# Performance work log

Hardware: AMD Instinct MI355X
Metric: run time of the kernel (lower is better)

The kernel has to match this reference:

```python
import jax, jax.numpy as jnp
import numpy as np

EMBED = 256

def _resize(x, h, w):
    # bilinear, half-pixel centers == torch align_corners=False
    B, C = x.shape[:2]
    return jax.image.resize(x, (B, C, h, w), method='bilinear')

def _conv(x, w, b, pad):
    y = jax.lax.conv_general_dilated(x, w, (1, 1), [(pad, pad), (pad, pad)],
                                     dimension_numbers=('NCHW', 'OIHW', 'NCHW'))
    return y + b[None, :, None, None]

def _box1d(x, r, axis):
    # windowed sum over [i-r, i+r], window clipped at borders
    x = jnp.moveaxis(x, axis, -1)
    n = x.shape[-1]
    c = jnp.cumsum(x, axis=-1)
    idx = jnp.arange(n)
    hi = c[..., jnp.clip(idx + r, 0, n - 1)]
    lo_i = idx - r - 1
    lo = jnp.where(lo_i >= 0, c[..., jnp.clip(lo_i, 0, n - 1)], 0.0)
    return jnp.moveaxis(hi - lo, -1, axis)

def _box_mean(x, r):
    # mean filter over (2r+1)^2 window, normalized by valid pixel count at borders
    H, W = x.shape[-2:]
    s = _box1d(_box1d(x, r, -2), r, -1)
    ch = _box1d(jnp.ones((H,), x.dtype), r, 0)
    cw = _box1d(jnp.ones((W,), x.dtype), r, 0)
    return s / (ch[:, None] * cw[None, :])

def _guided_filter(I, p, r, eps):
    # He et al. guided filter. I: (H,W) guide, p: (C,H,W) src, vectorized over C
    mean_I = _box_mean(I, r)
    var_I = _box_mean(I * I, r) - mean_I ** 2
    mean_p = _box_mean(p, r)
    cov_Ip = _box_mean(I[None] * p, r) - mean_I[None] * mean_p
    a = cov_Ip / (var_I[None] + eps)
    b = mean_p - a * mean_I[None]
    return _box_mean(a, r) * I[None] + _box_mean(b, r)

def _forward(fg, bg, mask, feat, w1, b1, w2, b2, w3, b3, wm, bm):
    h2, w2d = 2 * mask.shape[2], 2 * mask.shape[3]
    mask_2x_raw = _resize(mask, h2, w2d)
    feat_2x_raw = _resize(feat, h2, w2d)
    fg_2x = _resize(fg, h2, w2d)
    bg_2x = _resize(bg, h2, w2d)
    x = jnp.concatenate((mask_2x_raw, fg_2x, bg_2x, feat_2x_raw), axis=1)
    x = jax.nn.relu(_conv(x, w1, b1, 0))
    feat_2x = jax.nn.relu(_conv(x, w2, b2, 2))
    guide = jnp.mean(fg_2x, axis=1)[0] * 128.0  # (H2, W2)
    r = int(0.01 * h2)  # static shape -> python int, jit-safe
    filt = _guided_filter(guide, feat_2x[0], r, 0.01)[None]  # (1,C,H2,W2)
    feat_2x = jax.nn.relu(_conv(filt, w3, b3, 0))
    mask_2x = jax.nn.sigmoid(_conv(feat_2x, wm, bm, 0))
    return mask_2x, feat_2x

def setup_inputs():
    key = jax.random.key(0)
    ks = jax.random.split(key, 8)
    E = EMBED
    return {
        'fg': jax.random.normal(ks[0], (1, 3, 128, 128), jnp.float32),
        'bg': jax.random.normal(ks[1], (1, 3, 128, 128), jnp.float32),
        'mask': jax.random.uniform(ks[2], (1, 1, 128, 128), dtype=jnp.float32),
        'feat': jax.random.normal(ks[3], (1, E, 128, 128), jnp.float32),
        'w1': jax.random.normal(ks[4], (E, E + 7, 1, 1), jnp.float32) * 0.05,
        'b1': jnp.zeros((E,), jnp.float32),
        'w2': jax.random.normal(ks[5], (E, E, 5, 5), jnp.float32) * 0.02,
        'b2': jnp.zeros((E,), jnp.float32),
        'w3': jax.random.normal(ks[6], (E, E, 1, 1), jnp.float32) * 0.05,
        'b3': jnp.zeros((E,), jnp.float32),
        'wm': jax.random.normal(ks[7], (1, E, 1, 1), jnp.float32) * 0.05,
        'bm': jnp.zeros((1,), jnp.float32),
    }

def reference(fg, bg, mask, feat, w1, b1, w2, b2, w3, b3, wm, bm):
    return _forward(fg, bg, mask, feat, w1, b1, w2, b2, w3, b3, wm, bm)
```

## Files before the change

### kernel.cpp

```cpp
#include <hip/hip_runtime.h>
#include <hip/hip_bf16.h>
#include <math.h>


#define P2 65536
#define PADW 260

typedef short  frag8  __attribute__((ext_vector_type(8)));
typedef float  f32x4  __attribute__((ext_vector_type(4)));

__device__ __forceinline__ void load16_lds(const void* gsrc, void* lds) {
    __builtin_amdgcn_global_load_lds((const __attribute__((address_space(1))) void*)gsrc,
                                     (__attribute__((address_space(3))) void*)lds, 16, 0, 0);
}

struct BilC { int y0, y1, x0, x1; float wy0, wy1, wx0, wx1; };
__device__ __forceinline__ BilC bil_coords(int oy, int ox) {
    BilC c;
    int m = oy >> 1;
    if ((oy & 1) == 0) { c.y0 = (m > 0) ? m - 1 : 0; c.y1 = m; c.wy0 = 0.25f; }
    else               { c.y0 = m; c.y1 = (m < 127) ? m + 1 : 127; c.wy0 = 0.75f; }
    c.wy1 = 1.0f - c.wy0;
    int n = ox >> 1;
    if ((ox & 1) == 0) { c.x0 = (n > 0) ? n - 1 : 0; c.x1 = n; c.wx0 = 0.25f; }
    else               { c.x0 = n; c.x1 = (n < 127) ? n + 1 : 127; c.wx0 = 0.75f; }
    c.wx1 = 1.0f - c.wx0;
    return c;
}
__device__ __forceinline__ float bil_eval(const float* __restrict__ src, const BilC& c) {
    return c.wy0 * (c.wx0 * src[c.y0 * 128 + c.x0] + c.wx1 * src[c.y0 * 128 + c.x1])
         + c.wy1 * (c.wx0 * src[c.y1 * 128 + c.x0] + c.wx1 * src[c.y1 * 128 + c.x1]);
}

__global__ void upsample_x(const float* __restrict__ mask, const float* __restrict__ fg,
                           const float* __restrict__ bg, const float* __restrict__ feat,
                           __hip_bfloat16* __restrict__ xp) {
    int p = blockIdx.x * 256 + threadIdx.x;
    int chunk = blockIdx.y;
    union { __hip_bfloat16 h[8]; f32x4 v; } u;
    if (chunk >= 33) {
        f32x4 z = {0.f, 0.f, 0.f, 0.f};
        *(f32x4*)&xp[((size_t)chunk * P2 + p) * 8] = z;
        return;
    }
    BilC bc = bil_coords(p >> 8, p & 255);
#pragma unroll
    for (int j = 0; j < 8; j++) {
        int c = chunk * 8 + j;
        float v = 0.f;
        if (c < 263) {
            const float* src = (c == 0) ? mask
                             : (c < 4)  ? fg + (c - 1) * 16384
                             : (c < 7)  ? bg + (c - 4) * 16384
                             :            feat + (c - 7) * 16384;
            v = bil_eval(src, bc);
        }
        u.h[j] = __float2bfloat16(v);
    }
    *(f32x4*)&xp[((size_t)chunk * P2 + p) * 8] = u.v;
}

__global__ void guide_make(const float* __restrict__ fg, float* __restrict__ guide) {
    int p = blockIdx.x * 256 + threadIdx.x;
    BilC bc = bil_coords(p >> 8, p & 255);
    float s = bil_eval(fg, bc) + bil_eval(fg + 16384, bc) + bil_eval(fg + 32768, bc);
    guide[p] = s * (128.0f / 3.0f);
}

__global__ void gf_stats(const float* __restrict__ guide, float* __restrict__ meanI,
                         float* __restrict__ varI) {
    int p = blockIdx.x * 256 + threadIdx.x;
    int y = p >> 8, xq = p & 255;
    int y0 = (y - 2 > 0) ? y - 2 : 0, y1 = (y + 2 < 255) ? y + 2 : 255;
    int x0 = (xq - 2 > 0) ? xq - 2 : 0, x1 = (xq + 2 < 255) ? xq + 2 : 255;
    float s = 0.f, ss = 0.f;
    for (int yy = y0; yy <= y1; yy++)
        for (int xx = x0; xx <= x1; xx++) {
            float v = guide[yy * 256 + xx];
            s += v; ss += v * v;
        }
    float inv = 1.0f / (float)((y1 - y0 + 1) * (x1 - x0 + 1));
    float m = s * inv;
    meanI[p] = m;
    varI[p] = ss * inv - m * m;
}

__global__ void border_zero(__hip_bfloat16* __restrict__ y1p) {
    int idx = blockIdx.x * 256 + threadIdx.x;
    int p = idx >> 4;
    if (p >= PADW * PADW) return;
    int py = p / PADW, px = p - py * PADW;
    if (py >= 2 && py < 258 && px >= 2 && px < 258) return;
    f32x4 z = {0.f, 0.f, 0.f, 0.f};
    f32x4* dst = (f32x4*)&y1p[(size_t)p * 256 + (idx & 15) * 16];
    dst[0] = z; dst[1] = z;
}

__global__ void repack_1x1(const float* __restrict__ W, __hip_bfloat16* __restrict__ dst,
                           int K, int KT) {
    int idx = blockIdx.x * 256 + threadIdx.x;
    if (idx >= KT * 16 * 64) return;
    int lane = idx & 63;
    int nbg = (idx >> 6) & 15;
    int kt = idx >> 10;
    int oc = nbg * 16 + (lane & 15);
    int ic0 = kt * 32 + (lane >> 4) * 8;
    union { __hip_bfloat16 h[8]; f32x4 v; } u;
#pragma unroll
    for (int j = 0; j < 8; j++) {
        int ic = ic0 + j;
        u.h[j] = (ic < K) ? __float2bfloat16(W[(size_t)oc * K + ic]) : __float2bfloat16(0.f);
    }
    *(f32x4*)&dst[(size_t)idx * 8] = u.v;
}

__global__ void repack_w2(const float* __restrict__ w2, __hip_bfloat16* __restrict__ wpk) {
    int idx = blockIdx.x * 256 + threadIdx.x;
    int lane = idx & 63;
    int nb = (idx >> 6) & 15;
    int kt = (idx >> 10) & 7;
    int t  = idx >> 13;
    int oc = nb * 16 + (lane & 15);
    int ic0 = kt * 32 + (lane >> 4) * 8;
    union { __hip_bfloat16 h[8]; f32x4 v; } u;
#pragma unroll
    for (int j = 0; j < 8; j++)
        u.h[j] = __float2bfloat16(w2[(oc * 256 + ic0 + j) * 25 + t]);
    *(f32x4*)&wpk[(size_t)idx * 8] = u.v;
}

template<int MODE>
__global__ __launch_bounds__(256) void mfma_1x1(const __hip_bfloat16* __restrict__ xch,
                                                const __hip_bfloat16* __restrict__ wpk,
                                                const float* __restrict__ bias,
                                                void* __restrict__ outp, int KT) {
    __shared__ __align__(16) __hip_bfloat16 Asm[2][128 * 32];
    __shared__ __align__(16) __hip_bfloat16 Bsm[2][8 * 64 * 8];
    const int tid = threadIdx.x;
    const int wave = tid >> 6, lane = tid & 63;
    const int q = lane >> 4, m16 = lane & 15;
    const int wm = wave & 1, wn = wave >> 1;
    const int pb = blockIdx.x * 128, oh = blockIdx.y;

    f32x4 acc[4][4] = {};

    auto stA = [&](int kt, int buf) {
#pragma unroll
        for (int it = 0; it < 2; it++) {
            int chb = it * 256 + wave * 64;
            int ch = chb + lane;
            int px = ch >> 2, oct = ch & 3;
            const __hip_bfloat16* src = xch + ((size_t)(kt * 4 + oct) * P2 + pb + px) * 8;
            load16_lds(src, &Asm[buf][chb * 8]);
        }
    };
    auto stB = [&](int kt, int buf) {
#pragma unroll
        for (int it = 0; it < 2; it++) {
            int chb = it * 256 + wave * 64;
            int ch = chb + lane;
            int nb = ch >> 6, l = ch & 63;
            const __hip_bfloat16* src = wpk + (((size_t)kt * 16 + oh * 8 + nb) * 64 + l) * 8;
            load16_lds(src, &Bsm[buf][chb * 8]);
        }
    };
    stA(0, 0); stB(0, 0);
    int buf = 0;
    for (int kt = 0; kt < KT; kt++) {
        __syncthreads();
        if (kt + 1 < KT) { stA(kt + 1, buf ^ 1); stB(kt + 1, buf ^ 1); }
        frag8 a[4], b[4];
#pragma unroll
        for (int i = 0; i < 4; i++)
            a[i] = *(const frag8*)&Asm[buf][((wm * 4 + i) * 16 + m16) * 32 + q * 8];
#pragma unroll
        for (int j = 0; j < 4; j++)
            b[j] = *(const frag8*)&Bsm[buf][((wn * 4 + j) * 64 + lane) * 8];
#pragma unroll
        for (int i = 0; i < 4; i++)
#pragma unroll
            for (int j = 0; j < 4; j++)
                acc[i][j] = __builtin_amdgcn_mfma_f32_16x16x32_bf16(a[i], b[j], acc[i][j], 0, 0, 0);
        buf ^= 1;
    }
    if (MODE == 0) {
        __hip_bfloat16* y1p = (__hip_bfloat16*)outp;
#pragma unroll
        for (int j = 0; j < 4; j++) {
            int oc = oh * 128 + (wn * 4 + j) * 16 + m16;
            float bj = bias[oc];
#pragma unroll
            for (int i = 0; i < 4; i++) {
                f32x4 v = acc[i][j];
#pragma unroll
                for (int e = 0; e < 4; e++) {
                    int pix = pb + (wm * 4 + i) * 16 + q * 4 + e;
                    int py = pix >> 8, px = pix & 255;
                    float tv = v[e] + bj;
                    y1p[((size_t)(py + 2) * PADW + px + 2) * 256 + oc] =
                        __float2bfloat16(tv > 0.f ? tv : 0.f);
                }
            }
        }
    } else {
        float* out = (float*)outp;
#pragma unroll
        for (int j = 0; j < 4; j++) {
            int oc = oh * 128 + (wn * 4 + j) * 16 + m16;
            float bj = bias[oc];
#pragma unroll
            for (int i = 0; i < 4; i++) {
                f32x4 v = acc[i][j];
#pragma unroll
                for (int e = 0; e < 4; e++) { float tv = v[e] + bj; v[e] = tv > 0.f ? tv : 0.f; }
                *(f32x4*)&out[(size_t)oc * P2 + pb + (wm * 4 + i) * 16 + q * 4] = v;
            }
        }
    }
}

__global__ __launch_bounds__(128, 2) void conv5x5_mfma(const __hip_bfloat16* __restrict__ y1p,
                                                       const __hip_bfloat16* __restrict__ wpk,
                                                       const float* __restrict__ bias,
                                                       float* __restrict__ out) {
    __shared__ __align__(16) __hip_bfloat16 Asm[2][12 * 20 * 32];
    const int tid = threadIdx.x;
    const int wave = tid >> 6;
    const int lane = tid & 63;
    const int q = lane >> 4;
    const int m16 = lane & 15;
    const int bx = blockIdx.x, by = blockIdx.y, oh = blockIdx.z;

    f32x4 acc[4][8] = {};

    auto stageA = [&](int ict, int buf) {
#pragma unroll
        for (int g = 0; g < 8; g++) {
            int grp = g * 2 + wave;
            if (grp >= 15) break;
            int chb = grp * 64;
            int ch = chb + lane;
            int oct = ch & 3, pl = ch >> 2;
            int pc = pl % 20, pr = pl / 20;
            const __hip_bfloat16* src =
                y1p + (size_t)((by * 8 + pr) * PADW + bx * 16 + pc) * 256 + ict * 32 + oct * 8;
            load16_lds(src, &Asm[buf][chb * 8]);
        }
    };
    auto loadB = [&](int s, frag8* dst) {
        int ict = s / 25, tap = s - ict * 25;
        const __hip_bfloat16* base =
            wpk + ((size_t)((tap * 8 + ict) * 16 + oh * 8) * 64 + lane) * 8;
#pragma unroll
        for (int j = 0; j < 8; j++)
            dst[j] = *(const frag8*)(base + (size_t)j * 512);
    };

    frag8 bA[8], bB[8];
    stageA(0, 0);
    loadB(0, bA);
    int abuf = 0;

    auto step = [&](int s, frag8* bcur, frag8* bnxt) {
        int ict = s / 25, tap = s - ict * 25;
        if (tap == 0) __syncthreads();
        if (s + 1 < 200) loadB(s + 1, bnxt);
        if (tap == 24 && ict < 7) stageA(ict + 1, abuf ^ 1);
        int dy = tap / 5, dx = tap - dy * 5;
        frag8 a[4];
#pragma unroll
        for (int i = 0; i < 4; i++)
            a[i] = *(const frag8*)&Asm[abuf][((wave * 4 + i + dy) * 20 + m16 + dx) * 32 + q * 8];
#pragma unroll
        for (int i = 0; i < 4; i++)
#pragma unroll
            for (int j = 0; j < 8; j++)
                acc[i][j] = __builtin_amdgcn_mfma_f32_16x16x32_bf16(a[i], bcur[j], acc[i][j], 0, 0, 0);
        if (tap == 24) abuf ^= 1;
    };
    for (int s = 0; s < 200; s += 2) { step(s, bA, bB); step(s + 1, bB, bA); }

#pragma unroll
    for (int j = 0; j < 8; j++) {
        int oc = oh * 128 + j * 16 + m16;
        float bj = bias[oc];
#pragma unroll
        for (int i = 0; i < 4; i++) {
            int r = wave * 4 + i;
            f32x4 v = acc[i][j];
#pragma unroll
            for (int e = 0; e < 4; e++) {
                float t = v[e] + bj;
                v[e] = (t > 0.f) ? t : 0.f;
            }
            *(f32x4*)&out[(size_t)oc * P2 + (by * 8 + r) * 256 + bx * 16 + q * 4] = v;
        }
    }
}

__global__ __launch_bounds__(256) void gf_stream(const float* __restrict__ p,
                                                 const float* __restrict__ guide,
                                                 const float* __restrict__ meanI,
                                                 const float* __restrict__ varI,
                                                 __hip_bfloat16* __restrict__ filt) {
    __shared__ float Prow[260], IProw[260], Arow[260], Brow[260];
    const int t = threadIdx.x;
    const int c = blockIdx.y;
    const int Y0 = blockIdx.x * 64;
    const float* pc = p + (size_t)c * P2;
    if (t < 4) {
        int e = (t < 2) ? t : 256 + t;
        Prow[e] = 0.f; IProw[e] = 0.f; Arow[e] = 0.f; Brow[e] = 0.f;
    }
    int xlo = (t - 2 > 0) ? t - 2 : 0, xhi = (t + 2 < 255) ? t + 2 : 255;
    const float cxr = 1.0f / (float)(xhi - xlo + 1);
    float hp[5] = {0, 0, 0, 0, 0}, hip[5] = {0, 0, 0, 0, 0};
    float ha[5] = {0, 0, 0, 0, 0}, hb[5] = {0, 0, 0, 0, 0};
    float vp = 0.f, vip = 0.f, va = 0.f, vb = 0.f;
    __syncthreads();
    for (int s = 0; s < 72; s++) {
        int yL = Y0 - 4 + s;
        bool okL = ((unsigned)yL < 256u);
        if (okL) {
            float pv = pc[yL * 256 + t];
            Prow[t + 2] = pv;
            IProw[t + 2] = guide[yL * 256 + t] * pv;
        }
        __syncthreads();
        float hpn = 0.f, hipn = 0.f;
        if (okL) {
            hpn  = Prow[t] + Prow[t + 1] + Prow[t + 2] + Prow[t + 3] + Prow[t + 4];
            hipn = IProw[t] + IProw[t + 1] + IProw[t + 2] + IProw[t + 3] + IProw[t + 4];
        }
        vp += hpn - hp[0];  vip += hipn - hip[0];
        hp[0] = hp[1]; hp[1] = hp[2]; hp[2] = hp[3]; hp[3] = hp[4]; hp[4] = hpn;
        hip[0] = hip[1]; hip[1] = hip[2]; hip[2] = hip[3]; hip[3] = hip[4]; hip[4] = hipn;
        int yA = yL - 2;
        float aV = 0.f, bV = 0.f;
        if ((unsigned)yA < 256u && yA >= Y0 - 2) {
            int ylo = (yA - 2 > 0) ? yA - 2 : 0, yhi = (yA + 2 < 255) ? yA + 2 : 255;
            float inv1 = cxr / (float)(yhi - ylo + 1);
            float mI = meanI[yA * 256 + t], vI = varI[yA * 256 + t];
            float mp = vp * inv1, mip = vip * inv1;
            float cov = mip - mI * mp;
            aV = cov / (vI + 0.01f);
            bV = mp - aV * mI;
        }
        Arow[t + 2] = aV;
        Brow[t + 2] = bV;
        __syncthreads();
        float han = Arow[t] + Arow[t + 1] + Arow[t + 2] + Arow[t + 3] + Arow[t + 4];
        float hbn = Brow[t] + Brow[t + 1] + Brow[t + 2] + Brow[t + 3] + Brow[t + 4];
        va += han - ha[0];  vb += hbn - hb[0];
        ha[0] = ha[1]; ha[1] = ha[2]; ha[2] = ha[3]; ha[3] = ha[4]; ha[4] = han;
        hb[0] = hb[1]; hb[1] = hb[2]; hb[2] = hb[3]; hb[3] = hb[4]; hb[4] = hbn;
        int yo = yL - 4;
        if (yo >= Y0 && yo < Y0 + 64 && (unsigned)yo < 256u) {
            int ylo = (yo - 2 > 0) ? yo - 2 : 0, yhi = (yo + 2 < 255) ? yo + 2 : 255;
            float inv2 = cxr / (float)(yhi - ylo + 1);
            float I = guide[yo * 256 + t];
            filt[(size_t)c * P2 + yo * 256 + t] = __float2bfloat16((va * I + vb) * inv2);
        }
    }
}

__global__ void transpose_cp(const __hip_bfloat16* __restrict__ filt,
                             __hip_bfloat16* __restrict__ filtp) {
    __shared__ __hip_bfloat16 T[8][1024];
    int tid = threadIdx.x;
    int p0 = blockIdx.x * 1024;
    int cg = blockIdx.y;
    for (int i = tid; i < 8192; i += 256) {
        int r = i >> 10, pl = i & 1023;
        T[r][pl] = filt[(size_t)(cg * 8 + r) * P2 + p0 + pl];
    }
    __syncthreads();
    for (int pl = tid; pl < 1024; pl += 256) {
        union { __hip_bfloat16 h[8]; f32x4 v; } u;
#pragma unroll
        for (int j = 0; j < 8; j++) u.h[j] = T[j][pl];
        *(f32x4*)&filtp[((size_t)cg * P2 + p0 + pl) * 8] = u.v;
    }
}

__global__ void mask_head(const float* __restrict__ feat, const float* __restrict__ wm,
                          const float* __restrict__ bm, float* __restrict__ out) {
    int p = blockIdx.x * 256 + threadIdx.x;
    float acc = bm[0];
    for (int c = 0; c < 256; c++) acc += wm[c] * feat[(size_t)c * P2 + p];
    out[p] = 1.0f / (1.0f + expf(-acc));
}

extern "C" void kernel_launch(void* const* d_in, const int* in_sizes, int n_in,
                              void* d_out, int out_size, void* d_ws, size_t ws_size,
                              hipStream_t stream) {
    const float* fg   = (const float*)d_in[0];
    const float* bg   = (const float*)d_in[1];
    const float* mask = (const float*)d_in[2];
    const float* feat = (const float*)d_in[3];
    const float* w1   = (const float*)d_in[4];
    const float* b1   = (const float*)d_in[5];
    const float* w2   = (const float*)d_in[6];
    const float* b2   = (const float*)d_in[7];
    const float* w3   = (const float*)d_in[8];
    const float* b3   = (const float*)d_in[9];
    const float* wm   = (const float*)d_in[10];
    const float* bm   = (const float*)d_in[11];
    float* out = (float*)d_out;
    char* w8 = (char*)d_ws;

    float* pbuf = (float*)w8;
    __hip_bfloat16* xp    = (__hip_bfloat16*)(w8 + 67108864);
    __hip_bfloat16* filt  = (__hip_bfloat16*)(w8 + 67108864);
    __hip_bfloat16* filtp = (__hip_bfloat16*)w8;
    __hip_bfloat16* y1p   = (__hip_bfloat16*)(w8 + 104857600);
    __hip_bfloat16* wpk2  = (__hip_bfloat16*)(w8 + 139468800);
    __hip_bfloat16* wpk1  = (__hip_bfloat16*)(w8 + 142745600);
    __hip_bfloat16* wpk3  = (__hip_bfloat16*)(w8 + 142893056);
    float* guide = (float*)(w8 + 143024128);
    float* meanI = guide + P2;
    float* varI  = meanI + P2;

    upsample_x<<<dim3(256, 36), 256, 0, stream>>>(mask, fg, bg, feat, xp);
    guide_make<<<256, 256, 0, stream>>>(fg, guide);
    gf_stats<<<256, 256, 0, stream>>>(guide, meanI, varI);
    border_zero<<<4225, 256, 0, stream>>>(y1p);
    repack_w2<<<800, 256, 0, stream>>>(w2, wpk2);
    repack_1x1<<<36, 256, 0, stream>>>(w1, wpk1, 263, 9);
    repack_1x1<<<32, 256, 0, stream>>>(w3, wpk3, 256, 8);
    mfma_1x1<0><<<dim3(512, 2), 256, 0, stream>>>(xp, wpk1, b1, y1p, 9);
    conv5x5_mfma<<<dim3(16, 32, 2), 128, 0, stream>>>(y1p, wpk2, b2, pbuf);
    gf_stream<<<dim3(4, 256), 256, 0, stream>>>(pbuf, guide, meanI, varI, filt);
    transpose_cp<<<dim3(64, 32), 256, 0, stream>>>(filt, filtp);
    mfma_1x1<1><<<dim3(512, 2), 256, 0, stream>>>(filtp, wpk3, b3, out + P2, 8);
    mask_head<<<256, 256, 0, stream>>>(out + P2, wm, bm, out);
}
```

Baseline: 459.4 us.

## Fuse prep kernels, stage conv1 output via LDS, store conv5x5 output as fp16

Merges the border-zero and three weight-repack kernels into one launch. The first 1x1 conv epilogue now stages its tile in LDS so it can write 16-byte coalesced rows into the padded NHWC buffer instead of scattered 2-byte stores. The 5x5 conv writes its activation in fp16 rather than fp32, halving the traffic into the guided filter, and the mask head is vectorised to four pixels per thread. The fp16 intermediate adds rounding error before the guided filter.

```diff
diff --git a/kernel.cpp b/kernel.cpp
--- a/kernel.cpp
+++ b/kernel.cpp
@@ -1,5 +1,6 @@
 #include <hip/hip_runtime.h>
 #include <hip/hip_bf16.h>
+#include <hip/hip_fp16.h>
 #include <math.h>
 
 
@@ -85,48 +86,52 @@
     varI[p] = ss * inv - m * m;
 }
 
-__global__ void border_zero(__hip_bfloat16* __restrict__ y1p) {
-    int idx = blockIdx.x * 256 + threadIdx.x;
-    int p = idx >> 4;
-    if (p >= PADW * PADW) return;
-    int py = p / PADW, px = p - py * PADW;
-    if (py >= 2 && py < 258 && px >= 2 && px < 258) return;
-    f32x4 z = {0.f, 0.f, 0.f, 0.f};
-    f32x4* dst = (f32x4*)&y1p[(size_t)p * 256 + (idx & 15) * 16];
-    dst[0] = z; dst[1] = z;
-}
-
-__global__ void repack_1x1(const float* __restrict__ W, __hip_bfloat16* __restrict__ dst,
-                           int K, int KT) {
-    int idx = blockIdx.x * 256 + threadIdx.x;
-    if (idx >= KT * 16 * 64) return;
-    int lane = idx & 63;
-    int nbg = (idx >> 6) & 15;
-    int kt = idx >> 10;
-    int oc = nbg * 16 + (lane & 15);
-    int ic0 = kt * 32 + (lane >> 4) * 8;
-    union { __hip_bfloat16 h[8]; f32x4 v; } u;
-#pragma unroll
-    for (int j = 0; j < 8; j++) {
-        int ic = ic0 + j;
-        u.h[j] = (ic < K) ? __float2bfloat16(W[(size_t)oc * K + ic]) : __float2bfloat16(0.f);
-    }
-    *(f32x4*)&dst[(size_t)idx * 8] = u.v;
-}
-
-__global__ void repack_w2(const float* __restrict__ w2, __hip_bfloat16* __restrict__ wpk) {
-    int idx = blockIdx.x * 256 + threadIdx.x;
-    int lane = idx & 63;
-    int nb = (idx >> 6) & 15;
-    int kt = (idx >> 10) & 7;
-    int t  = idx >> 13;
-    int oc = nb * 16 + (lane & 15);
-    int ic0 = kt * 32 + (lane >> 4) * 8;
-    union { __hip_bfloat16 h[8]; f32x4 v; } u;
-#pragma unroll
-    for (int j = 0; j < 8; j++)
-        u.h[j] = __float2bfloat16(w2[(oc * 256 + ic0 + j) * 25 + t]);
-    *(f32x4*)&wpk[(size_t)idx * 8] = u.v;
+__global__ void prep_all(const float* __restrict__ w2, const float* __restrict__ w1,
+                         const float* __restrict__ w3,
+                         __hip_bfloat16* __restrict__ wpk2, __hip_bfloat16* __restrict__ wpk1,
+                         __hip_bfloat16* __restrict__ wpk3, __hip_bfloat16* __restrict__ y1p) {
+    int b = blockIdx.x;
+    int tid = threadIdx.x;
+    if (b < 4225) {
+        int idx = b * 256 + tid;
+        int p = idx >> 4;
+        if (p >= PADW * PADW) return;
+        int py = p / PADW, px = p - py * PADW;
+        if (py >= 2 && py < 258 && px >= 2 && px < 258) return;
+        f32x4 z = {0.f, 0.f, 0.f, 0.f};
+        f32x4* dst = (f32x4*)&y1p[(size_t)p * 256 + (idx & 15) * 16];
+        dst[0] = z; dst[1] = z;
+    } else if (b < 5025) {
+        int idx = (b - 4225) * 256 + tid;
+        int lane = idx & 63;
+        int nb = (idx >> 6) & 15;
+        int kt = (idx >> 10) & 7;
+        int t  = idx >> 13;
+        int oc = nb * 16 + (lane & 15);
+        int ic0 = kt * 32 + (lane >> 4) * 8;
+        union { __hip_bfloat16 h[8]; f32x4 v; } u;
+#pragma unroll
+        for (int j = 0; j < 8; j++)
+            u.h[j] = __float2bfloat16(w2[(oc * 256 + ic0 + j) * 25 + t]);
+        *(f32x4*)&wpk2[(size_t)idx * 8] = u.v;
+    } else {
+        const float* W; __hip_bfloat16* dst; int K, KT, idx;
+        if (b < 5061) { W = w1; dst = wpk1; K = 263; KT = 9; idx = (b - 5025) * 256 + tid; }
+        else          { W = w3; dst = wpk3; K = 256; KT = 8; idx = (b - 5061) * 256 + tid; }
+        if (idx >= KT * 16 * 64) return;
+        int lane = idx & 63;
+        int nbg = (idx >> 6) & 15;
+        int kt = idx >> 10;
+        int oc = nbg * 16 + (lane & 15);
+        int ic0 = kt * 32 + (lane >> 4) * 8;
+        union { __hip_bfloat16 h[8]; f32x4 v; } u;
+#pragma unroll
+        for (int j = 0; j < 8; j++) {
+            int ic = ic0 + j;
+            u.h[j] = (ic < K) ? __float2bfloat16(W[(size_t)oc * K + ic]) : __float2bfloat16(0.f);
+        }
+        *(f32x4*)&dst[(size_t)idx * 8] = u.v;
+    }
 }
 
 template<int MODE>
@@ -134,8 +139,9 @@
                                                 const __hip_bfloat16* __restrict__ wpk,
                                                 const float* __restrict__ bias,
                                                 void* __restrict__ outp, int KT) {
-    __shared__ __align__(16) __hip_bfloat16 Asm[2][128 * 32];
-    __shared__ __align__(16) __hip_bfloat16 Bsm[2][8 * 64 * 8];
+    __shared__ __align__(16) char smem[MODE == 0 ? 34816 : 32768];
+    __hip_bfloat16* Asm0 = (__hip_bfloat16*)smem;
+    __hip_bfloat16* Bsm0 = (__hip_bfloat16*)(smem + 16384);
     const int tid = threadIdx.x;
     const int wave = tid >> 6, lane = tid & 63;
     const int q = lane >> 4, m16 = lane & 15;
@@ -151,7 +157,7 @@
             int ch = chb + lane;
             int px = ch >> 2, oct = ch & 3;
             const __hip_bfloat16* src = xch + ((size_t)(kt * 4 + oct) * P2 + pb + px) * 8;
-            load16_lds(src, &Asm[buf][chb * 8]);
+            load16_lds(src, &Asm0[(size_t)buf * 4096 + chb * 8]);
         }
     };
     auto stB = [&](int kt, int buf) {
@@ -161,7 +167,7 @@
             int ch = chb + lane;
             int nb = ch >> 6, l = ch & 63;
             const __hip_bfloat16* src = wpk + (((size_t)kt * 16 + oh * 8 + nb) * 64 + l) * 8;
-            load16_lds(src, &Bsm[buf][chb * 8]);
+            load16_lds(src, &Bsm0[(size_t)buf * 4096 + chb * 8]);
         }
     };
     stA(0, 0); stB(0, 0);
@@ -172,10 +178,10 @@
         frag8 a[4], b[4];
 #pragma unroll
         for (int i = 0; i < 4; i++)
-            a[i] = *(const frag8*)&Asm[buf][((wm * 4 + i) * 16 + m16) * 32 + q * 8];
+            a[i] = *(const frag8*)&Asm0[(size_t)buf * 4096 + ((wm * 4 + i) * 16 + m16) * 32 + q * 8];
 #pragma unroll
         for (int j = 0; j < 4; j++)
-            b[j] = *(const frag8*)&Bsm[buf][((wn * 4 + j) * 64 + lane) * 8];
+            b[j] = *(const frag8*)&Bsm0[(size_t)buf * 4096 + ((wn * 4 + j) * 64 + lane) * 8];
 #pragma unroll
         for (int i = 0; i < 4; i++)
 #pragma unroll
@@ -184,7 +190,36 @@
         buf ^= 1;
     }
     if (MODE == 0) {
+        __syncthreads();
+        __hip_bfloat16* Ct = (__hip_bfloat16*)smem;
+#pragma unroll
+        for (int j = 0; j < 4; j++) {
+            int ocr = (wn * 4 + j) * 16 + m16;
+            float bj = bias[oh * 128 + ocr];
+#pragma unroll
+            for (int i = 0; i < 4; i++) {
+                f32x4 v = acc[i][j];
+#pragma unroll
+                for (int e = 0; e < 4; e++) {
+                    int pxr = (wm * 4 + i) * 16 + q * 4 + e;
+                    float tv = v[e] + bj;
+                    Ct[pxr * 136 + ocr] = __float2bfloat16(tv > 0.f ? tv : 0.f);
+                }
+            }
+        }
+        __syncthreads();
         __hip_bfloat16* y1p = (__hip_bfloat16*)outp;
+        int colr = (tid & 15) * 8;
+#pragma unroll
+        for (int it = 0; it < 8; it++) {
+            int pxr = it * 16 + (tid >> 4);
+            int pix = pb + pxr;
+            int py = pix >> 8, px = pix & 255;
+            f32x4 val = *(f32x4*)&Ct[pxr * 136 + colr];
+            *(f32x4*)&y1p[((size_t)(py + 2) * PADW + px + 2) * 256 + oh * 128 + colr] = val;
+        }
+    } else {
+        float* out = (float*)outp;
 #pragma unroll
         for (int j = 0; j < 4; j++) {
             int oc = oh * 128 + (wn * 4 + j) * 16 + m16;
@@ -193,25 +228,6 @@
             for (int i = 0; i < 4; i++) {
                 f32x4 v = acc[i][j];
 #pragma unroll
-                for (int e = 0; e < 4; e++) {
-                    int pix = pb + (wm * 4 + i) * 16 + q * 4 + e;
-                    int py = pix >> 8, px = pix & 255;
-                    float tv = v[e] + bj;
-                    y1p[((size_t)(py + 2) * PADW + px + 2) * 256 + oc] =
-                        __float2bfloat16(tv > 0.f ? tv : 0.f);
-                }
-            }
-        }
-    } else {
-        float* out = (float*)outp;
-#pragma unroll
-        for (int j = 0; j < 4; j++) {
-            int oc = oh * 128 + (wn * 4 + j) * 16 + m16;
-            float bj = bias[oc];
-#pragma unroll
-            for (int i = 0; i < 4; i++) {
-                f32x4 v = acc[i][j];
-#pragma unroll
                 for (int e = 0; e < 4; e++) { float tv = v[e] + bj; v[e] = tv > 0.f ? tv : 0.f; }
                 *(f32x4*)&out[(size_t)oc * P2 + pb + (wm * 4 + i) * 16 + q * 4] = v;
             }
@@ -222,7 +238,7 @@
 __global__ __launch_bounds__(128, 2) void conv5x5_mfma(const __hip_bfloat16* __restrict__ y1p,
                                                        const __hip_bfloat16* __restrict__ wpk,
                                                        const float* __restrict__ bias,
-                                                       float* __restrict__ out) {
+                                                       __half* __restrict__ pf) {
     __shared__ __align__(16) __hip_bfloat16 Asm[2][12 * 20 * 32];
     const int tid = threadIdx.x;
     const int wave = tid >> 6;
@@ -288,17 +304,18 @@
         for (int i = 0; i < 4; i++) {
             int r = wave * 4 + i;
             f32x4 v = acc[i][j];
+            union { __half h[4]; double d; } u;
 #pragma unroll
             for (int e = 0; e < 4; e++) {
                 float t = v[e] + bj;
-                v[e] = (t > 0.f) ? t : 0.f;
+                u.h[e] = __float2half(t > 0.f ? t : 0.f);
             }
-            *(f32x4*)&out[(size_t)oc * P2 + (by * 8 + r) * 256 + bx * 16 + q * 4] = v;
-        }
-    }
-}
-
-__global__ __launch_bounds__(256) void gf_stream(const float* __restrict__ p,
+            *(double*)&pf[(size_t)oc * P2 + (by * 8 + r) * 256 + bx * 16 + q * 4] = u.d;
+        }
+    }
+}
+
+__global__ __launch_bounds__(256) void gf_stream(const __half* __restrict__ p,
                                                  const float* __restrict__ guide,
                                                  const float* __restrict__ meanI,
                                                  const float* __restrict__ varI,
@@ -307,7 +324,7 @@
     const int t = threadIdx.x;
     const int c = blockIdx.y;
     const int Y0 = blockIdx.x * 64;
-    const float* pc = p + (size_t)c * P2;
+    const __half* pc = p + (size_t)c * P2;
     if (t < 4) {
         int e = (t < 2) ? t : 256 + t;
         Prow[e] = 0.f; IProw[e] = 0.f; Arow[e] = 0.f; Brow[e] = 0.f;
@@ -322,7 +339,7 @@
         int yL = Y0 - 4 + s;
         bool okL = ((unsigned)yL < 256u);
         if (okL) {
-            float pv = pc[yL * 256 + t];
+            float pv = __half2float(pc[yL * 256 + t]);
             Prow[t + 2] = pv;
             IProw[t + 2] = guide[yL * 256 + t] * pv;
         }
@@ -385,10 +402,19 @@
 
 __global__ void mask_head(const float* __restrict__ feat, const float* __restrict__ wm,
                           const float* __restrict__ bm, float* __restrict__ out) {
-    int p = blockIdx.x * 256 + threadIdx.x;
-    float acc = bm[0];
-    for (int c = 0; c < 256; c++) acc += wm[c] * feat[(size_t)c * P2 + p];
-    out[p] = 1.0f / (1.0f + expf(-acc));
+    int p4 = (blockIdx.x * 256 + threadIdx.x) * 4;
+    float b0 = bm[0];
+    f32x4 acc = {b0, b0, b0, b0};
+    for (int c = 0; c < 256; c++) {
+        f32x4 v = *(const f32x4*)&feat[(size_t)c * P2 + p4];
+        float w = wm[c];
+#pragma unroll
+        for (int e = 0; e < 4; e++) acc[e] += w * v[e];
+    }
+    f32x4 r;
+#pragma unroll
+    for (int e = 0; e < 4; e++) r[e] = 1.0f / (1.0f + expf(-acc[e]));
+    *(f32x4*)&out[p4] = r;
 }
 
 extern "C" void kernel_launch(void* const* d_in, const int* in_sizes, int n_in,
@@ -409,10 +435,10 @@
     float* out = (float*)d_out;
     char* w8 = (char*)d_ws;
 
-    float* pbuf = (float*)w8;
+    __half* pbuf          = (__half*)w8;
+    __hip_bfloat16* filtp = (__hip_bfloat16*)(w8 + 33554432);
     __hip_bfloat16* xp    = (__hip_bfloat16*)(w8 + 67108864);
     __hip_bfloat16* filt  = (__hip_bfloat16*)(w8 + 67108864);
-    __hip_bfloat16* filtp = (__hip_bfloat16*)w8;
     __hip_bfloat16* y1p   = (__hip_bfloat16*)(w8 + 104857600);
     __hip_bfloat16* wpk2  = (__hip_bfloat16*)(w8 + 139468800);
     __hip_bfloat16* wpk1  = (__hip_bfloat16*)(w8 + 142745600);
@@ -424,14 +450,11 @@
     upsample_x<<<dim3(256, 36), 256, 0, stream>>>(mask, fg, bg, feat, xp);
     guide_make<<<256, 256, 0, stream>>>(fg, guide);
     gf_stats<<<256, 256, 0, stream>>>(guide, meanI, varI);
-    border_zero<<<4225, 256, 0, stream>>>(y1p);
-    repack_w2<<<800, 256, 0, stream>>>(w2, wpk2);
-    repack_1x1<<<36, 256, 0, stream>>>(w1, wpk1, 263, 9);
-    repack_1x1<<<32, 256, 0, stream>>>(w3, wpk3, 256, 8);
+    prep_all<<<5093, 256, 0, stream>>>(w2, w1, w3, wpk2, wpk1, wpk3, y1p);
     mfma_1x1<0><<<dim3(512, 2), 256, 0, stream>>>(xp, wpk1, b1, y1p, 9);
     conv5x5_mfma<<<dim3(16, 32, 2), 128, 0, stream>>>(y1p, wpk2, b2, pbuf);
     gf_stream<<<dim3(4, 256), 256, 0, stream>>>(pbuf, guide, meanI, varI, filt);
     transpose_cp<<<dim3(64, 32), 256, 0, stream>>>(filt, filtp);
     mfma_1x1<1><<<dim3(512, 2), 256, 0, stream>>>(filtp, wpk3, b3, out + P2, 8);
-    mask_head<<<256, 256, 0, stream>>>(out + P2, wm, bm, out);
-}
+    mask_head<<<64, 256, 0, stream>>>(out + P2, wm, bm, out);
+}
```

Measured after the change: 442.3 us. -3.7%, faster.
